# Kernel optimization log

Measured on AMD Instinct MI355X. Metric: run time of the kernel, lower is better.

The kernel has to match this reference:

```python
import jax, jax.numpy as jnp
import numpy as np

GRID = 385  # (W+1) = (H+1) = (D+1) corners of a 384^3 voxel grid


def setup_inputs() -> dict:
    key = jax.random.key(0)
    occ = jax.random.uniform(key, (GRID, GRID, GRID), dtype=jnp.float32)
    return {"occ": occ}


def reference(occ):
    # Occupancy connectivity loss: sum over axis-aligned neighbor pairs of
    # |occ_i - occ_j| (each pair counted once via the 3 forward directions).
    lx = jnp.sum(jnp.abs(occ[1:, :, :] - occ[:-1, :, :]))
    ly = jnp.sum(jnp.abs(occ[:, 1:, :] - occ[:, :-1, :]))
    lz = jnp.sum(jnp.abs(occ[:, :, 1:] - occ[:, :, :-1]))
    return lx + ly + lz
```

## Files before the change

kernel.cpp:

```cpp
#include <hip/hip_runtime.h>


constexpr int G     = 385;
constexpr int PLANE = G * G;

#define TPB  256
#define ZT   3
#define YT   12
#define XC   64
#define NBLK (ZT * YT * XC)
#define S    148

typedef float f4v __attribute__((ext_vector_type(4)));
static __device__ __forceinline__ f4v ld4(const float* p) { return *(const f4v*)p; }

__global__ __launch_bounds__(TPB) void occ_conn_main(
    const float* __restrict__ a, float* __restrict__ ws)
{
    __shared__ float T[2][33][S];
    float s = 0.f;

    const int tz = threadIdx.x & 31;
    const int ty = threadIdx.x >> 5;

    int t = blockIdx.x;
    const int bc = t % XC;  t /= XC;
    const int by = t % YT;  t /= YT;
    const int bz = t;
    const unsigned gy0 = by * 32u;
    const unsigned gz0 = bz * 128u;
    const int  P0    = bc * 6;
    const bool lastc = (bc == XC - 1);
    const bool ey    = (by == YT - 1);
    const bool ez    = (bz == ZT - 1);

    f4v m0, m1, m2, m3, h;

    for (int tt = 0; tt <= 7; ++tt) {
        const int x = P0 + tt;

        if (tt <= 6) {
            const unsigned base = (unsigned)x * (unsigned)PLANE + gy0 * (unsigned)G + gz0;
            const unsigned W0 = base + (unsigned)ty * (unsigned)G;
            const unsigned W1 = W0 +  8u * (unsigned)G;
            const unsigned W2 = W0 + 16u * (unsigned)G;
            const unsigned W3 = W0 + 24u * (unsigned)G;
            m0 = ld4(a + (W0 - (W0 & 3u)) + 4u * (unsigned)tz);
            m1 = ld4(a + (W1 - (W1 & 3u)) + 4u * (unsigned)tz);
            m2 = ld4(a + (W2 - (W2 & 3u)) + 4u * (unsigned)tz);
            m3 = ld4(a + (W3 - (W3 & 3u)) + 4u * (unsigned)tz);
            if (ty == 0) {
                const unsigned W32 = base + 32u * (unsigned)G;
                h = ld4(a + (W32 - (W32 & 3u)) + 4u * (unsigned)tz);
            } else if (ty == 1) {
                const unsigned Wr = base + (unsigned)tz * (unsigned)G;
                h = ld4(a + (Wr - (Wr & 3u)) + 128u);
            } else if (ty == 2 && tz == 0) {
                const unsigned W32 = base + 32u * (unsigned)G;
                h = ld4(a + (W32 - (W32 & 3u)) + 128u);
            }
        }

        if (tt >= 1) {
            const int xc = x - 1;
            const float (*C)[S]  = T[(tt - 1) & 1];
            const float (*Pv)[S] = T[tt & 1];
            const bool zy = (tt <= 6) || (lastc && tt == 7);
            const bool xd = (tt >= 2);

            #pragma unroll
            for (int rr = 0; rr < 4; ++rr) {
                const int r = ty + 8 * rr;
                const unsigned phi  = (unsigned)(xc + (int)gy0 + r) & 3u;
                const unsigned phin = (phi + 1u) & 3u;
                const unsigned phip = (phi + 3u) & 3u;
                #pragma unroll
                for (int j = 0; j < 4; ++j) {
                    const int zl = tz + 32 * j;
                    const float v = C[r][phi + zl];
                    if (zy) {
                        s += fabsf(C[r][phi + zl + 1] - v);
                        s += fabsf(C[r + 1][phin + zl] - v);
                    }
                    if (xd) s += fabsf(v - Pv[r][phip + zl]);
                }
            }

            if (ez && ty == 4) {
                const int r = tz;
                const unsigned phi  = (unsigned)(xc + (int)gy0 + r) & 3u;
                const unsigned phin = (phi + 1u) & 3u;
                const unsigned phip = (phi + 3u) & 3u;
                const float v = C[r][phi + 128];
                if (zy) s += fabsf(C[r + 1][phin + 128] - v);
                if (xd) s += fabsf(v - Pv[r][phip + 128]);
            }
            if (ey && ty == 5) {
                const unsigned phi  = (unsigned)(xc + (int)gy0 + 32) & 3u;
                const unsigned phip = (phi + 3u) & 3u;
                #pragma unroll
                for (int j = 0; j < 4; ++j) {
                    const int zl = tz + 32 * j;
                    const float v = C[32][phi + zl];
                    if (zy) s += fabsf(C[32][phi + zl + 1] - v);
                    if (xd) s += fabsf(v - Pv[32][phip + zl]);
                }
            }
            if (ey && ez && ty == 6 && tz == 0 && xd) {
                const unsigned phi  = (unsigned)(xc + (int)gy0 + 32) & 3u;
                const unsigned phip = (phi + 3u) & 3u;
                s += fabsf(C[32][phi + 128] - Pv[32][phip + 128]);
            }
        }

        __syncthreads();

        if (tt <= 6) {
            float (*B)[S] = T[tt & 1];
            *(f4v*)&B[ty +  0][4 * tz] = m0;
            *(f4v*)&B[ty +  8][4 * tz] = m1;
            *(f4v*)&B[ty + 16][4 * tz] = m2;
            *(f4v*)&B[ty + 24][4 * tz] = m3;
            if      (ty == 0)            *(f4v*)&B[32][4 * tz] = h;
            else if (ty == 1)            *(f4v*)&B[tz][128]    = h;
            else if (ty == 2 && tz == 0) *(f4v*)&B[32][128]    = h;
        }
        __syncthreads();
    }

    #pragma unroll
    for (int off = 32; off > 0; off >>= 1) s += __shfl_down(s, off, 64);
    __shared__ float ls[TPB / 64];
    const int lane = threadIdx.x & 63;
    const int wid  = threadIdx.x >> 6;
    if (lane == 0) ls[wid] = s;
    __syncthreads();
    if (threadIdx.x == 0) {
        float tsum = 0.f;
        #pragma unroll
        for (int w = 0; w < TPB / 64; ++w) tsum += ls[w];
        ws[blockIdx.x] = tsum;
    }
}

__global__ __launch_bounds__(256) void occ_conn_final(
    const float* __restrict__ ws, float* __restrict__ out)
{
    float s = 0.f;
    for (int i = threadIdx.x; i < NBLK; i += 256) s += ws[i];
    #pragma unroll
    for (int off = 32; off > 0; off >>= 1) s += __shfl_down(s, off, 64);
    __shared__ float ls[4];
    const int lane = threadIdx.x & 63;
    const int wid  = threadIdx.x >> 6;
    if (lane == 0) ls[wid] = s;
    __syncthreads();
    if (threadIdx.x == 0) out[0] = ls[0] + ls[1] + ls[2] + ls[3];
}

extern "C" void kernel_launch(void* const* d_in, const int* in_sizes, int n_in,
                              void* d_out, int out_size, void* d_ws, size_t ws_size,
                              hipStream_t stream)
{
    const float* a   = (const float*)d_in[0];
    float*       out = (float*)d_out;
    float*       ws  = (float*)d_ws;

    occ_conn_main<<<NBLK, TPB, 0, stream>>>(a, ws);
    occ_conn_final<<<1, 256, 0, stream>>>(ws, out);
}
```

Before: 318.4 us.

## Stream longer x-chunks with register-held previous plane and shuffle z-neighbours

Each block now walks 24 x-planes instead of 6, cutting the block count and the number of halo planes reloaded at chunk boundaries. The previous plane stays in registers, so x-differences no longer read shared memory. Loads become unaligned float4 reads, which removes the phase-offset indexing. z-neighbour differences use in-lane vector elements plus a wavefront shuffle, and one __syncthreads per iteration is dropped by relying on the double buffer. The trade-off is fewer blocks (576) and therefore less parallelism across CUs, plus more register pressure.

Measured after the change: 316.7 us. About the same (-0.6%).

```diff
diff --git a/kernel.cpp b/kernel.cpp
--- a/kernel.cpp
+++ b/kernel.cpp
@@ -4,15 +4,21 @@
 constexpr int G     = 385;
 constexpr int PLANE = G * G;
 
-#define TPB  256
-#define ZT   3
-#define YT   12
-#define XC   64
-#define NBLK (ZT * YT * XC)
-#define S    148
+#define TPB   256
+#define ZT    3
+#define YT    12
+#define XC    16
+#define XP    24
+#define NBLK  (ZT * YT * XC)
+#define S     140
 
 typedef float f4v __attribute__((ext_vector_type(4)));
-static __device__ __forceinline__ f4v ld4(const float* p) { return *(const f4v*)p; }
+
+static __device__ __forceinline__ f4v ldg4u(const float* __restrict__ p) {
+    f4v r;
+    __builtin_memcpy(&r, p, sizeof(r));
+    return r;
+}
 
 __global__ __launch_bounds__(TPB) void occ_conn_main(
     const float* __restrict__ a, float* __restrict__ ws)
@@ -29,101 +35,89 @@
     const int bz = t;
     const unsigned gy0 = by * 32u;
     const unsigned gz0 = bz * 128u;
-    const int  P0    = bc * 6;
+    const int  P0    = bc * XP;
     const bool lastc = (bc == XC - 1);
     const bool ey    = (by == YT - 1);
     const bool ez    = (bz == ZT - 1);
+    const int  TMAX  = lastc ? XP + 1 : XP;
 
-    f4v m0, m1, m2, m3, h;
+    f4v m0, m1, m2, m3;
+    f4v p0, p1, p2, p3;
+    f4v h, hp;
+    float h2 = 0.f, h2p = 0.f;
 
-    for (int tt = 0; tt <= 7; ++tt) {
-        const int x = P0 + tt;
+    const float* rowp = a + ((unsigned)P0 * (unsigned)PLANE + gy0 * (unsigned)G + gz0);
 
-        if (tt <= 6) {
-            const unsigned base = (unsigned)x * (unsigned)PLANE + gy0 * (unsigned)G + gz0;
-            const unsigned W0 = base + (unsigned)ty * (unsigned)G;
-            const unsigned W1 = W0 +  8u * (unsigned)G;
-            const unsigned W2 = W0 + 16u * (unsigned)G;
-            const unsigned W3 = W0 + 24u * (unsigned)G;
-            m0 = ld4(a + (W0 - (W0 & 3u)) + 4u * (unsigned)tz);
-            m1 = ld4(a + (W1 - (W1 & 3u)) + 4u * (unsigned)tz);
-            m2 = ld4(a + (W2 - (W2 & 3u)) + 4u * (unsigned)tz);
-            m3 = ld4(a + (W3 - (W3 & 3u)) + 4u * (unsigned)tz);
+    for (int tt = 0; tt <= TMAX; ++tt) {
+        if (tt <= XP) {
+            const float* rp = rowp + 4u * (unsigned)tz;
+            m0 = ldg4u(rp + (unsigned)(ty     ) * G);
+            m1 = ldg4u(rp + (unsigned)(ty +  8) * G);
+            m2 = ldg4u(rp + (unsigned)(ty + 16) * G);
+            m3 = ldg4u(rp + (unsigned)(ty + 24) * G);
             if (ty == 0) {
-                const unsigned W32 = base + 32u * (unsigned)G;
-                h = ld4(a + (W32 - (W32 & 3u)) + 4u * (unsigned)tz);
+                h = ldg4u(rowp + 32u * G + 4u * (unsigned)tz);
             } else if (ty == 1) {
-                const unsigned Wr = base + (unsigned)tz * (unsigned)G;
-                h = ld4(a + (Wr - (Wr & 3u)) + 128u);
+                h[0] = rowp[(unsigned)tz * G + 128u];
             } else if (ty == 2 && tz == 0) {
-                const unsigned W32 = base + 32u * (unsigned)G;
-                h = ld4(a + (W32 - (W32 & 3u)) + 128u);
+                h2 = rowp[32u * G + 128u];
             }
         }
 
         if (tt >= 1) {
-            const int xc = x - 1;
-            const float (*C)[S]  = T[(tt - 1) & 1];
-            const float (*Pv)[S] = T[tt & 1];
-            const bool zy = (tt <= 6) || (lastc && tt == 7);
-            const bool xd = (tt >= 2);
+            const float (*C)[S] = T[(tt - 1) & 1];
+            const bool xd = (tt <= XP);
 
             #pragma unroll
             for (int rr = 0; rr < 4; ++rr) {
                 const int r = ty + 8 * rr;
-                const unsigned phi  = (unsigned)(xc + (int)gy0 + r) & 3u;
-                const unsigned phin = (phi + 1u) & 3u;
-                const unsigned phip = (phi + 3u) & 3u;
-                #pragma unroll
-                for (int j = 0; j < 4; ++j) {
-                    const int zl = tz + 32 * j;
-                    const float v = C[r][phi + zl];
-                    if (zy) {
-                        s += fabsf(C[r][phi + zl + 1] - v);
-                        s += fabsf(C[r + 1][phin + zl] - v);
-                    }
-                    if (xd) s += fabsf(v - Pv[r][phip + zl]);
-                }
+                const f4v v = rr == 0 ? p0 : rr == 1 ? p1 : rr == 2 ? p2 : p3;
+                s += fabsf(v[1] - v[0]) + fabsf(v[2] - v[1]) + fabsf(v[3] - v[2]);
+                float zb = __shfl_down(v[0], 1);
+                if (tz == 31) zb = C[r][128];
+                s += fabsf(zb - v[3]);
+                const f4v yn = *(const f4v*)&C[r + 1][4 * tz];
+                s += fabsf(yn[0] - v[0]) + fabsf(yn[1] - v[1])
+                   + fabsf(yn[2] - v[2]) + fabsf(yn[3] - v[3]);
             }
 
-            if (ez && ty == 4) {
-                const int r = tz;
-                const unsigned phi  = (unsigned)(xc + (int)gy0 + r) & 3u;
-                const unsigned phin = (phi + 1u) & 3u;
-                const unsigned phip = (phi + 3u) & 3u;
-                const float v = C[r][phi + 128];
-                if (zy) s += fabsf(C[r + 1][phin + 128] - v);
-                if (xd) s += fabsf(v - Pv[r][phip + 128]);
+            if (ey && ty == 0) {
+                s += fabsf(hp[1] - hp[0]) + fabsf(hp[2] - hp[1]) + fabsf(hp[3] - hp[2]);
+                float zb = __shfl_down(hp[0], 1);
+                if (tz == 31) zb = C[32][128];
+                s += fabsf(zb - hp[3]);
             }
-            if (ey && ty == 5) {
-                const unsigned phi  = (unsigned)(xc + (int)gy0 + 32) & 3u;
-                const unsigned phip = (phi + 3u) & 3u;
+            if (ez && ty == 1) {
+                s += fabsf(C[tz + 1][128] - hp[0]);
+            }
+
+            if (xd) {
                 #pragma unroll
-                for (int j = 0; j < 4; ++j) {
-                    const int zl = tz + 32 * j;
-                    const float v = C[32][phi + zl];
-                    if (zy) s += fabsf(C[32][phi + zl + 1] - v);
-                    if (xd) s += fabsf(v - Pv[32][phip + zl]);
+                for (int rr = 0; rr < 4; ++rr) {
+                    const f4v v = rr == 0 ? p0 : rr == 1 ? p1 : rr == 2 ? p2 : p3;
+                    const f4v w = rr == 0 ? m0 : rr == 1 ? m1 : rr == 2 ? m2 : m3;
+                    s += fabsf(w[0] - v[0]) + fabsf(w[1] - v[1])
+                       + fabsf(w[2] - v[2]) + fabsf(w[3] - v[3]);
                 }
-            }
-            if (ey && ez && ty == 6 && tz == 0 && xd) {
-                const unsigned phi  = (unsigned)(xc + (int)gy0 + 32) & 3u;
-                const unsigned phip = (phi + 3u) & 3u;
-                s += fabsf(C[32][phi + 128] - Pv[32][phip + 128]);
+                if (ey && ty == 0)
+                    s += fabsf(h[0] - hp[0]) + fabsf(h[1] - hp[1])
+                       + fabsf(h[2] - hp[2]) + fabsf(h[3] - hp[3]);
+                if (ez && ty == 1)                        s += fabsf(h[0] - hp[0]);
+                if (ey && ez && ty == 2 && tz == 0)       s += fabsf(h2 - h2p);
             }
         }
 
-        __syncthreads();
-
-        if (tt <= 6) {
+        if (tt <= XP) {
             float (*B)[S] = T[tt & 1];
-            *(f4v*)&B[ty +  0][4 * tz] = m0;
+            *(f4v*)&B[ty      ][4 * tz] = m0;
             *(f4v*)&B[ty +  8][4 * tz] = m1;
             *(f4v*)&B[ty + 16][4 * tz] = m2;
             *(f4v*)&B[ty + 24][4 * tz] = m3;
             if      (ty == 0)            *(f4v*)&B[32][4 * tz] = h;
-            else if (ty == 1)            *(f4v*)&B[tz][128]    = h;
-            else if (ty == 2 && tz == 0) *(f4v*)&B[32][128]    = h;
+            else if (ty == 1)            B[tz][128] = h[0];
+            else if (ty == 2 && tz == 0) B[32][128] = h2;
+            p0 = m0; p1 = m1; p2 = m2; p3 = m3; hp = h; h2p = h2;
+            rowp += PLANE;
         }
         __syncthreads();
     }
```
